# Performance work log

Measured on AMD Instinct MI355X. Metric: run time of the kernel, lower is better.

Reference implementation:

```python
import jax, jax.numpy as jnp
import numpy as np

SLOPE = 0.1
EPS = 1e-5


def setup_inputs() -> dict:
    key = jax.random.key(0)
    ks = jax.random.split(key, 12)
    C, INTER, RED = 256, 128, 32
    B, H, W = 8, 128, 128
    s = 0.05
    return {
        "x": jax.random.normal(ks[0], (B, C, H, W), jnp.float32),
        "se_w1": jax.random.normal(ks[1], (RED, C), jnp.float32) * s,
        "se_w2": jax.random.normal(ks[2], (C, RED), jnp.float32) * s,
        "wq": jax.random.normal(ks[3], (INTER, C), jnp.float32) * s,
        "bq": jax.random.normal(ks[4], (INTER,), jnp.float32) * s,
        "wk": jax.random.normal(ks[5], (INTER, C), jnp.float32) * s,
        "bk": jax.random.normal(ks[6], (INTER,), jnp.float32) * s,
        "wv": jax.random.normal(ks[7], (INTER, C), jnp.float32) * s,
        "bv": jax.random.normal(ks[8], (INTER,), jnp.float32) * s,
        "w_wg": jax.random.normal(ks[9], (INTER, INTER), jnp.float32) * s,
        "g_wg": jnp.ones((INTER,), jnp.float32),
        "be_wg": jnp.zeros((INTER,), jnp.float32),
        "rm_wg": jnp.zeros((INTER,), jnp.float32),
        "rv_wg": jnp.ones((INTER,), jnp.float32),
        "w_out": jax.random.normal(ks[10], (C, INTER), jnp.float32) * s,
        "b_out": jax.random.normal(ks[11], (C,), jnp.float32) * s,
        "g_out": jnp.ones((C,), jnp.float32),
        "be_out": jnp.zeros((C,), jnp.float32),
        "rm_out": jnp.zeros((C,), jnp.float32),
        "rv_out": jnp.ones((C,), jnp.float32),
    }


def _bn(x, g, b, rm, rv):
    # eval-mode batch norm over channel axis 1; x: [b, c, ...]
    shape = (1, -1) + (1,) * (x.ndim - 2)
    inv = g / jnp.sqrt(rv + EPS)
    return x * inv.reshape(shape) + (b - rm * inv).reshape(shape)


def reference(x, se_w1, se_w2, wq, bq, wk, bk, wv, bv,
              w_wg, g_wg, be_wg, rm_wg, rv_wg,
              w_out, b_out, g_out, be_out, rm_out, rv_out):
    B, C, H, W = x.shape
    # ---- Speactral_Attention (SE block) ----
    y = x.mean(axis=(2, 3))                                  # [b, c]
    y = jax.nn.leaky_relu(y @ se_w1.T, SLOPE)                # [b, c//8]
    y = jax.nn.sigmoid(y @ se_w2.T)                          # [b, c]
    xs = x * y[:, :, None, None]
    # ---- Spatial_GR ----
    xf = xs.reshape(B, C, H * W)                             # [b, c, n]
    q = jnp.einsum('ic,bcn->bin', wq, xf) + bq[None, :, None]
    k = jnp.einsum('ic,bcn->bin', wk, xf) + bk[None, :, None]
    v = jnp.einsum('ic,bcn->bin', wv, xf) + bv[None, :, None]
    # AV = softmax(q @ v^T) over last dim: [b, i, i]
    att = jax.nn.softmax(jnp.einsum('bin,bjn->bij', q, v), axis=2)
    # bmm(k^T, att) then transpose -> av[b,i,n] = sum_j att[b,j,i] * k[b,j,n]
    av = jnp.einsum('bji,bjn->bin', att, k)                  # [b, inter, n]
    avw = jnp.einsum('oi,bin->bon', w_wg, av)                # conv1d k=1, no bias
    avw = _bn(avw, g_wg, be_wg, rm_wg, rv_wg)
    out = jnp.einsum('co,bon->bcn', w_out, avw) + b_out[None, :, None]
    out = _bn(out.reshape(B, C, H, W), g_out, be_out, rm_out, rv_out)
    return jax.nn.leaky_relu(out + xs, SLOPE)
```

## Files before the change

### kernel.cpp

```cpp
#include <hip/hip_runtime.h>
#include <hip/hip_fp16.h>

#define NPIX 16384
#define CCH 256
#define INTR 128
#define REDD 32
#define NB 8
#define SLOPE 0.1f
#define BNEPS 1e-5f

typedef _Float16 f16x8 __attribute__((ext_vector_type(8)));
typedef __attribute__((ext_vector_type(16))) float f32x16;

#define OFF_GX    0
#define OFF_YM    524288
#define OFF_SC    526336
#define OFF_QS    530432
#define OFF_VS    531456
#define OFF_SWG   532480
#define OFF_TWG   532608
#define OFF_SOUT  532736
#define OFF_TOUT  532992
#define OFF_M     795392
#define OFF_W7    1450752
#define OFF_B6    1975040
#define OFF_XH    1977088
#define OFF_PART  18754304

__device__ __forceinline__ unsigned short h1(float f) {
    __half h = __float2half(f);
    return __half_as_ushort(h);
}

__device__ __forceinline__ uint4 cvt8h(const float4 a, const float4 c) {
    __half2 p0 = __floats2half2_rn(a.x, a.y);
    __half2 p1 = __floats2half2_rn(a.z, a.w);
    __half2 p2 = __floats2half2_rn(c.x, c.y);
    __half2 p3 = __floats2half2_rn(c.z, c.w);
    uint4 r;
    r.x = *(unsigned int*)&p0; r.y = *(unsigned int*)&p1;
    r.z = *(unsigned int*)&p2; r.w = *(unsigned int*)&p3;
    return r;
}

__device__ __forceinline__ f16x8 cvt8hf(const float4 a, const float4 c) {
    uint4 u = cvt8h(a, c);
    return *(f16x8*)&u;
}

__device__ __forceinline__ void gload_lds16(const void* g, void* l) {
    __builtin_amdgcn_global_load_lds((const __attribute__((address_space(1))) void*)g,
                                     (__attribute__((address_space(3))) void*)l, 16, 0, 0);
}

__global__ __launch_bounds__(256) void cvtrow_kernel(const float* __restrict__ x,
                                                     unsigned short* __restrict__ xh,
                                                     float* __restrict__ ymsum) {
    int row = blockIdx.x;
    const float4* p4 = (const float4*)(x + (size_t)row * NPIX);
    uint4* o4 = (uint4*)(xh + (size_t)row * NPIX);
    float s = 0.f;
    for (int i = threadIdx.x; i < NPIX / 8; i += 256) {
        float4 v0 = p4[2 * i];
        float4 v1 = p4[2 * i + 1];
        s += (v0.x + v0.y) + (v0.z + v0.w) + (v1.x + v1.y) + (v1.z + v1.w);
        o4[i] = cvt8h(v0, v1);
    }
    for (int off = 32; off > 0; off >>= 1) s += __shfl_xor(s, off);
    __shared__ float red[4];
    if ((threadIdx.x & 63) == 0) red[threadIdx.x >> 6] = s;
    __syncthreads();
    if (threadIdx.x == 0)
        ymsum[row] = red[0] + red[1] + red[2] + red[3];
}

__global__ __launch_bounds__(256) void head_kernel(const float* __restrict__ ymsum,
                                                   const float* __restrict__ se_w1,
                                                   const float* __restrict__ se_w2,
                                                   const float* __restrict__ wq,
                                                   const float* __restrict__ wv,
                                                   const float* __restrict__ g_wg, const float* __restrict__ be_wg,
                                                   const float* __restrict__ rm_wg, const float* __restrict__ rv_wg,
                                                   const float* __restrict__ g_out, const float* __restrict__ be_out,
                                                   const float* __restrict__ rm_out, const float* __restrict__ rv_out,
                                                   float* __restrict__ scale,
                                                   float* __restrict__ qs, float* __restrict__ vs,
                                                   float* __restrict__ swg, float* __restrict__ twg,
                                                   float* __restrict__ sout, float* __restrict__ tout) {
    int b = blockIdx.x, t = threadIdx.x;
    __shared__ float ys[CCH], y1s[REDD], rs[CCH];
    float ymr = ymsum[b * CCH + t];
    ys[t] = ymr * (1.f / 16384.f);
    if (b == 0) {
        if (t < INTR) {
            float s = g_wg[t] / sqrtf(rv_wg[t] + BNEPS);
            swg[t] = s;
            twg[t] = be_wg[t] - rm_wg[t] * s;
        }
        float s = g_out[t] / sqrtf(rv_out[t] + BNEPS);
        sout[t] = s;
        tout[t] = be_out[t] - rm_out[t] * s;
    }
    __syncthreads();
    if (t < REDD) {
        float a = 0.f;
        #pragma unroll 4
        for (int c = 0; c < CCH; ++c) a += se_w1[t * CCH + c] * ys[c];
        y1s[t] = a > 0.f ? a : SLOPE * a;
    }
    __syncthreads();
    float a = 0.f;
    #pragma unroll
    for (int r = 0; r < REDD; ++r) a += se_w2[t * REDD + r] * y1s[r];
    float sg = 1.f / (1.f + expf(-a));
    scale[b * CCH + t] = sg;
    rs[t] = sg * ymr;
    __syncthreads();
    const float* w = (t < INTR) ? (wq + t * CCH) : (wv + (t - INTR) * CCH);
    float a2 = 0.f;
    #pragma unroll 4
    for (int c = 0; c < CCH; ++c) a2 += w[c] * rs[c];
    if (t < INTR) qs[b * INTR + t] = a2;
    else          vs[b * INTR + (t - INTR)] = a2;
}

__global__ __launch_bounds__(256) void gram_partial_kernel(const unsigned short* __restrict__ xh,
                                                           unsigned short* __restrict__ partials,
                                                           int nch) {
    __shared__ __align__(16) unsigned short Ah[128 * 64];
    __shared__ __align__(16) unsigned short Bh[128 * 64];
    int bid = blockIdx.x;
    int chunk = bid % nch;
    int t2 = bid / nch;
    int tile = t2 % 3;
    int b = t2 / 3;
    int rowbase = (tile == 1) ? 128 : 0;
    int colbase = (tile == 0) ? 0 : 128;
    bool diag = (tile < 2);
    const unsigned short* xb = xh + (size_t)b * CCH * NPIX;
    int kpb = NPIX / nch;
    int n0 = chunk * kpb;
    int nsteps = kpb >> 6;
    int tid = threadIdx.x;
    int l = tid & 63, w = tid >> 6;
    int wrow = (w >> 1) * 64, wcol = (w & 1) * 64;
    int sr = l >> 3, ssg = l & 7;

    f32x16 acc[2][2];
    #pragma unroll
    for (int i = 0; i < 2; ++i)
        #pragma unroll
        for (int j = 0; j < 2; ++j)
            #pragma unroll
            for (int r = 0; r < 16; ++r) acc[i][j][r] = 0.f;

    for (int step = 0; step < nsteps; ++step) {
        int k0 = n0 + step * 64;
        __syncthreads();
        #pragma unroll
        for (int e = 0; e < 4; ++e) {
            int rbase = e * 32 + w * 8;
            int r = rbase + sr;
            int seg = ssg ^ (r & 7);
            gload_lds16(&xb[(size_t)(rowbase + r) * NPIX + k0 + seg * 8], &Ah[rbase * 64]);
            if (!diag)
                gload_lds16(&xb[(size_t)(colbase + r) * NPIX + k0 + seg * 8], &Bh[rbase * 64]);
        }
        __syncthreads();
        const unsigned short* BP = diag ? Ah : Bh;
        #pragma unroll
        for (int kk = 0; kk < 4; ++kk) {
            int useg = kk * 2 + (l >> 5);
            f16x8 af[2], bf[2];
            #pragma unroll
            for (int at = 0; at < 2; ++at) {
                int r = wrow + at * 32 + (l & 31);
                af[at] = *(const f16x8*)&Ah[r * 64 + ((useg ^ (r & 7)) << 3)];
            }
            #pragma unroll
            for (int bt = 0; bt < 2; ++bt) {
                int c = wcol + bt * 32 + (l & 31);
                bf[bt] = *(const f16x8*)&BP[c * 64 + ((useg ^ (c & 7)) << 3)];
            }
            #pragma unroll
            for (int at = 0; at < 2; ++at)
                #pragma unroll
                for (int bt = 0; bt < 2; ++bt)
                    acc[at][bt] = __builtin_amdgcn_mfma_f32_32x32x16_f16(af[at], bf[bt], acc[at][bt], 0, 0, 0);
        }
    }
    unsigned short* P = partials + (size_t)bid * (128 * 128);
    #pragma unroll
    for (int at = 0; at < 2; ++at)
        #pragma unroll
        for (int bt = 0; bt < 2; ++bt)
            #pragma unroll
            for (int r = 0; r < 16; ++r) {
                int lr = wrow + at * 32 + (r & 3) + ((r >> 2) << 3) + ((l >> 5) << 2);
                int lc = wcol + bt * 32 + (l & 31);
                P[lr * 128 + lc] = h1(acc[at][bt][r]);
            }
}

__global__ __launch_bounds__(256) void gram_reduce_kernel(const unsigned short* __restrict__ partials,
                                                          float* __restrict__ Gx,
                                                          int nch) {
    int bid = blockIdx.x;
    int part = bid & 15;
    int tileIdx = bid >> 4;
    int tile = tileIdx % 3;
    int b = tileIdx / 3;
    int rowbase = (tile == 1) ? 128 : 0;
    int colbase = (tile == 0) ? 0 : 128;
    int locIdx = part * 1024 + threadIdx.x * 4;
    const unsigned short* P = partials + (size_t)tileIdx * nch * (128 * 128) + locIdx;
    float4 s = make_float4(0.f, 0.f, 0.f, 0.f);
    for (int ch = 0; ch < nch; ++ch) {
        ushort4 v = *(const ushort4*)(P + (size_t)ch * (128 * 128));
        s.x += __half2float(__ushort_as_half(v.x));
        s.y += __half2float(__ushort_as_half(v.y));
        s.z += __half2float(__ushort_as_half(v.z));
        s.w += __half2float(__ushort_as_half(v.w));
    }
    int lr = locIdx >> 7, lc = locIdx & 127;
    float* G = Gx + (size_t)b * CCH * CCH;
    *(float4*)&G[(rowbase + lr) * CCH + colbase + lc] = s;
    if (tile == 2) {
        G[(colbase + lc + 0) * CCH + rowbase + lr] = s.x;
        G[(colbase + lc + 1) * CCH + rowbase + lr] = s.y;
        G[(colbase + lc + 2) * CCH + rowbase + lr] = s.z;
        G[(colbase + lc + 3) * CCH + rowbase + lr] = s.w;
    }
}

__global__ __launch_bounds__(256) void ts_kernel(const float* __restrict__ wq,
                                                 const float* __restrict__ scale,
                                                 const float* __restrict__ Gx,
                                                 const float* __restrict__ wv,
                                                 const float* __restrict__ bq,
                                                 const float* __restrict__ bv,
                                                 const float* __restrict__ qs,
                                                 const float* __restrict__ vs,
                                                 float* __restrict__ M) {
    int bid = blockIdx.x;
    int i = bid & 127, b = bid >> 7;
    int t = threadIdx.x;
    __shared__ float sw[CCH];
    __shared__ float t1s[CCH];
    __shared__ float part[256];
    __shared__ float redm[2], reds[2];
    sw[t] = wq[i * CCH + t] * scale[b * CCH + t];
    __syncthreads();
    const float* G = Gx + (size_t)b * CCH * CCH;
    float acc = 0.f;
    #pragma unroll 4
    for (int c = 0; c < CCH; ++c) acc += sw[c] * G[c * CCH + t];
    t1s[t] = acc * scale[b * CCH + t];
    __syncthreads();
    int j = t & 127, h = t >> 7;
    const float* wvr = wv + j * CCH + h * 128;
    const float* tp = t1s + h * 128;
    float p = 0.f;
    #pragma unroll 4
    for (int c = 0; c < 128; ++c) p += tp[c] * wvr[c];
    part[t] = p;
    __syncthreads();
    float acc2 = 0.f;
    if (t < 128)
        acc2 = part[t] + part[t + 128]
             + bq[i] * vs[b * INTR + j] + bv[j] * qs[b * INTR + i] + 16384.f * bq[i] * bv[j];
    float m = acc2;
    for (int off = 32; off > 0; off >>= 1) m = fmaxf(m, __shfl_xor(m, off));
    if (t == 0) redm[0] = m;
    if (t == 64) redm[1] = m;
    __syncthreads();
    m = fmaxf(redm[0], redm[1]);
    float e = expf(acc2 - m);
    float s = e;
    for (int off = 32; off > 0; off >>= 1) s += __shfl_xor(s, off);
    if (t == 0) reds[0] = s;
    if (t == 64) reds[1] = s;
    __syncthreads();
    s = reds[0] + reds[1];
    if (t < 128)
        M[(size_t)b * INTR * INTR + j * INTR + i] = e / s;
}

__global__ __launch_bounds__(256) void tail_kernel(const float* __restrict__ M,
                                                   const float* __restrict__ wk,
                                                   const float* __restrict__ bk,
                                                   const float* __restrict__ wwg,
                                                   const float* __restrict__ swg,
                                                   const float* __restrict__ twg,
                                                   const float* __restrict__ wout,
                                                   const float* __restrict__ bout,
                                                   const float* __restrict__ sout,
                                                   const float* __restrict__ tout,
                                                   const float* __restrict__ scale,
                                                   unsigned short* __restrict__ W7h,
                                                   float* __restrict__ b6) {
    __shared__ __align__(16) unsigned short Bt[256 * 128];
    __shared__ __align__(16) unsigned short Ot[256 * 128];
    __shared__ float bavS[INTR], b2S[INTR], scS[CCH], soS[CCH], swgS[INTR];
    int b = blockIdx.x, tid = threadIdx.x;
    int l = tid & 63, w = tid >> 6;
    const float* Mb = M + (size_t)b * INTR * INTR;

    scS[tid] = scale[b * CCH + tid];
    soS[tid] = sout[tid];
    if (tid < INTR) swgS[tid] = swg[tid];

    {
        int mn = tid & 63;
        int mk0 = tid >> 6;
        #pragma unroll
        for (int e = 0; e < 8; ++e) {
            int j0 = (mk0 + 4 * e) * 4;
            int c0 = mn * 4;
            float4 q0 = *(const float4*)&wk[(size_t)(j0 + 0) * CCH + c0];
            float4 q1 = *(const float4*)&wk[(size_t)(j0 + 1) * CCH + c0];
            float4 q2 = *(const float4*)&wk[(size_t)(j0 + 2) * CCH + c0];
            float4 q3 = *(const float4*)&wk[(size_t)(j0 + 3) * CCH + c0];
            int unit = j0 >> 3, sub = (j0 >> 2) & 1;
            int key = (c0 >> 2) & 7;
            #pragma unroll
            for (int jj = 0; jj < 4; ++jj) {
                float e0 = jj == 0 ? q0.x : jj == 1 ? q0.y : jj == 2 ? q0.z : q0.w;
                float e1 = jj == 0 ? q1.x : jj == 1 ? q1.y : jj == 2 ? q1.z : q1.w;
                float e2 = jj == 0 ? q2.x : jj == 1 ? q2.y : jj == 2 ? q2.z : q2.w;
                float e3 = jj == 0 ? q3.x : jj == 1 ? q3.y : jj == 2 ? q3.z : q3.w;
                ushort4 cv = make_ushort4(h1(e0), h1(e1), h1(e2), h1(e3));
                *(ushort4*)&Bt[(c0 + jj) * 128 + ((unit ^ key) << 3) + sub * 4] = cv;
            }
        }
    }
    if (tid < INTR) {
        float a = 0.f;
        #pragma unroll 4
        for (int j = 0; j < INTR; ++j) a += Mb[tid * INTR + j] * bk[j];
        bavS[tid] = a;
    }
    __syncthreads();

    {
        f32x16 acc[4][2];
        #pragma unroll
        for (int at = 0; at < 4; ++at)
            #pragma unroll
            for (int bt = 0; bt < 2; ++bt)
                #pragma unroll
                for (int r = 0; r < 16; ++r) acc[at][bt][r] = 0.f;
        #pragma unroll
        for (int kk = 0; kk < 8; ++kk) {
            int useg = kk * 2 + (l >> 5);
            f16x8 bf[2];
            #pragma unroll
            for (int bt = 0; bt < 2; ++bt) {
                int c = w * 64 + bt * 32 + (l & 31);
                bf[bt] = *(const f16x8*)&Bt[c * 128 + ((useg ^ ((c >> 2) & 7)) << 3)];
            }
            #pragma unroll
            for (int at = 0; at < 4; ++at) {
                int i = at * 32 + (l & 31);
                float4 a0 = *(const float4*)&Mb[(size_t)i * INTR + useg * 8];
                float4 a1 = *(const float4*)&Mb[(size_t)i * INTR + useg * 8 + 4];
                f16x8 af = cvt8hf(a0, a1);
                #pragma unroll
                for (int bt = 0; bt < 2; ++bt)
                    acc[at][bt] = __builtin_amdgcn_mfma_f32_32x32x16_f16(af, bf[bt], acc[at][bt], 0, 0, 0);
            }
        }
        if (tid < INTR) {
            float a = 0.f;
            #pragma unroll 4
            for (int i = 0; i < INTR; ++i) a += wwg[tid * INTR + i] * bavS[i];
            b2S[tid] = swgS[tid] * a + twg[tid];
        }
        __syncthreads();
        #pragma unroll
        for (int at = 0; at < 4; ++at)
            #pragma unroll
            for (int bt = 0; bt < 2; ++bt)
                #pragma unroll
                for (int r = 0; r < 16; ++r) {
                    int i = at * 32 + (r & 3) + ((r >> 2) << 3) + ((l >> 5) << 2);
                    int c = w * 64 + bt * 32 + (l & 31);
                    Ot[c * 128 + (((i >> 3) ^ ((c >> 2) & 7)) << 3) + (i & 7)] = h1(acc[at][bt][r]);
                }
    }
    __syncthreads();

    {
        f32x16 acc[4][2];
        #pragma unroll
        for (int at = 0; at < 4; ++at)
            #pragma unroll
            for (int bt = 0; bt < 2; ++bt)
                #pragma unroll
                for (int r = 0; r < 16; ++r) acc[at][bt][r] = 0.f;
        #pragma unroll
        for (int kk = 0; kk < 8; ++kk) {
            int useg = kk * 2 + (l >> 5);
            f16x8 bf[2];
            #pragma unroll
            for (int bt = 0; bt < 2; ++bt) {
                int c = w * 64 + bt * 32 + (l & 31);
                bf[bt] = *(const f16x8*)&Ot[c * 128 + ((useg ^ ((c >> 2) & 7)) << 3)];
            }
            #pragma unroll
            for (int at = 0; at < 4; ++at) {
                int o = at * 32 + (l & 31);
                float4 a0 = *(const float4*)&wwg[(size_t)o * INTR + useg * 8];
                float4 a1 = *(const float4*)&wwg[(size_t)o * INTR + useg * 8 + 4];
                f16x8 af = cvt8hf(a0, a1);
                #pragma unroll
                for (int bt = 0; bt < 2; ++bt)
                    acc[at][bt] = __builtin_amdgcn_mfma_f32_32x32x16_f16(af, bf[bt], acc[at][bt], 0, 0, 0);
            }
        }
        {
            float a = 0.f;
            #pragma unroll 4
            for (int o = 0; o < INTR; ++o) a += wout[tid * INTR + o] * b2S[o];
            float b5 = a + bout[tid];
            b6[b * CCH + tid] = soS[tid] * b5 + tout[tid];
        }
        __syncthreads();
        #pragma unroll
        for (int at = 0; at < 4; ++at)
            #pragma unroll
            for (int bt = 0; bt < 2; ++bt)
                #pragma unroll
                for (int r = 0; r < 16; ++r) {
                    int o = at * 32 + (r & 3) + ((r >> 2) << 3) + ((l >> 5) << 2);
                    int c = w * 64 + bt * 32 + (l & 31);
                    Bt[c * 128 + (((o >> 3) ^ ((c >> 2) & 7)) << 3) + (o & 7)] = h1(swgS[o] * acc[at][bt][r]);
                }
    }
    __syncthreads();

    unsigned short* Wb = W7h + (size_t)b * CCH * CCH;
    #pragma unroll
    for (int p = 0; p < 2; ++p) {
        f32x16 acc[4][2];
        #pragma unroll
        for (int at = 0; at < 4; ++at)
            #pragma unroll
            for (int bt = 0; bt < 2; ++bt)
                #pragma unroll
                for (int r = 0; r < 16; ++r) acc[at][bt][r] = 0.f;
        #pragma unroll
        for (int kk = 0; kk < 8; ++kk) {
            int useg = kk * 2 + (l >> 5);
            f16x8 bf[2];
            #pragma unroll
            for (int bt = 0; bt < 2; ++bt) {
                int cp = w * 64 + bt * 32 + (l & 31);
                bf[bt] = *(const f16x8*)&Bt[cp * 128 + ((useg ^ ((cp >> 2) & 7)) << 3)];
            }
            #pragma unroll
            for (int at = 0; at < 4; ++at) {
                int cc = p * 128 + at * 32 + (l & 31);
                float4 a0 = *(const float4*)&wout[(size_t)cc * INTR + useg * 8];
                float4 a1 = *(const float4*)&wout[(size_t)cc * INTR + useg * 8 + 4];
                f16x8 af = cvt8hf(a0, a1);
                #pragma unroll
                for (int bt = 0; bt < 2; ++bt)
                    acc[at][bt] = __builtin_amdgcn_mfma_f32_32x32x16_f16(af, bf[bt], acc[at][bt], 0, 0, 0);
            }
        }
        #pragma unroll
        for (int at = 0; at < 4; ++at)
            #pragma unroll
            for (int bt = 0; bt < 2; ++bt)
                #pragma unroll
                for (int r = 0; r < 16; ++r) {
                    int c = p * 128 + at * 32 + (r & 3) + ((r >> 2) << 3) + ((l >> 5) << 2);
                    int cp = w * 64 + bt * 32 + (l & 31);
                    float w6 = soS[c] * acc[at][bt][r] + ((c == cp) ? 1.f : 0.f);
                    Wb[c * CCH + cp] = h1(w6 * scS[cp]);
                }
    }
}

__global__ __launch_bounds__(256, 4) void final_mfma_kernel(const unsigned short* __restrict__ W7h,
                                                            const unsigned short* __restrict__ xh,
                                                            const float* __restrict__ b6,
                                                            float* __restrict__ out) {
    __shared__ __align__(16) unsigned short Ws[128 * 64];
    __shared__ __align__(16) unsigned short Xs[128 * 64];
    int bid0 = blockIdx.x;
    int bid = (bid0 & 7) * 256 + (bid0 >> 3);
    int ct = bid & 1;
    int nt = (bid >> 1) & 127;
    int b = bid >> 8;
    int cbase = ct * 128, n0 = nt * 128;
    const unsigned short* xb = xh + (size_t)b * CCH * NPIX;
    const unsigned short* Wb = W7h + (size_t)b * CCH * CCH;
    int tid = threadIdx.x;
    int l = tid & 63, w = tid >> 6;
    int wrow = (w >> 1) * 64, wcol = (w & 1) * 64;
    int mn = tid & 31, mk0 = tid >> 5;
    int sr = l >> 3, ssg = l & 7;

    f32x16 acc[2][2];
    #pragma unroll
    for (int i = 0; i < 2; ++i)
        #pragma unroll
        for (int j = 0; j < 2; ++j)
            #pragma unroll
            for (int r = 0; r < 16; ++r) acc[i][j][r] = 0.f;

    for (int step = 0; step < 4; ++step) {
        int k0 = step * 64;
        __syncthreads();
        #pragma unroll
        for (int e = 0; e < 4; ++e) {
            int rbase = e * 32 + w * 8;
            int r = rbase + sr;
            int seg = ssg ^ (r & 7);
            gload_lds16(&Wb[(size_t)(cbase + r) * CCH + k0 + seg * 8], &Ws[rbase * 64]);
        }
        #pragma unroll
        for (int mi = 0; mi < 2; ++mi) {
            int mk = mk0 + mi * 8;
            const unsigned short* sp = &xb[(size_t)(k0 + mk * 4) * NPIX + n0 + mn * 4];
            ushort4 q0 = *(const ushort4*)sp;
            ushort4 q1 = *(const ushort4*)(sp + NPIX);
            ushort4 q2 = *(const ushort4*)(sp + 2 * NPIX);
            ushort4 q3 = *(const ushort4*)(sp + 3 * NPIX);
            int klo = mk * 4;
            int unit = klo >> 3, sub = (klo & 7) >> 2;
            #pragma unroll
            for (int j = 0; j < 4; ++j) {
                unsigned short e0 = j == 0 ? q0.x : j == 1 ? q0.y : j == 2 ? q0.z : q0.w;
                unsigned short e1 = j == 0 ? q1.x : j == 1 ? q1.y : j == 2 ? q1.z : q1.w;
                unsigned short e2 = j == 0 ? q2.x : j == 1 ? q2.y : j == 2 ? q2.z : q2.w;
                unsigned short e3 = j == 0 ? q3.x : j == 1 ? q3.y : j == 2 ? q3.z : q3.w;
                int nl = mn * 4 + j;
                ushort4 cv = make_ushort4(e0, e1, e2, e3);
                int idx = nl * 64 + ((unit ^ ((nl >> 2) & 7)) << 3) + sub * 4;
                *(ushort4*)&Xs[idx] = cv;
            }
        }
        __syncthreads();
        #pragma unroll
        for (int kk = 0; kk < 4; ++kk) {
            int useg = kk * 2 + (l >> 5);
            f16x8 af[2], bfr[2];
            #pragma unroll
            for (int at = 0; at < 2; ++at) {
                int c = wrow + at * 32 + (l & 31);
                af[at] = *(const f16x8*)&Ws[c * 64 + ((useg ^ (c & 7)) << 3)];
            }
            #pragma unroll
            for (int bt = 0; bt < 2; ++bt) {
                int n = wcol + bt * 32 + (l & 31);
                bfr[bt] = *(const f16x8*)&Xs[n * 64 + ((useg ^ ((n >> 2) & 7)) << 3)];
            }
            #pragma unroll
            for (int at = 0; at < 2; ++at)
                #pragma unroll
                for (int bt = 0; bt < 2; ++bt)
                    acc[at][bt] = __builtin_amdgcn_mfma_f32_32x32x16_f16(af[at], bfr[bt], acc[at][bt], 0, 0, 0);
        }
    }
    #pragma unroll
    for (int at = 0; at < 2; ++at)
        #pragma unroll
        for (int bt = 0; bt < 2; ++bt)
            #pragma unroll
            for (int r = 0; r < 16; ++r) {
                int c = cbase + wrow + at * 32 + (r & 3) + ((r >> 2) << 3) + ((l >> 5) << 2);
                int n = n0 + wcol + bt * 32 + (l & 31);
                float v = acc[at][bt][r] + b6[b * CCH + c];
                v = v > 0.f ? v : SLOPE * v;
                out[(size_t)b * CCH * NPIX + (size_t)c * NPIX + n] = v;
            }
}

extern "C" void kernel_launch(void* const* d_in, const int* in_sizes, int n_in,
                              void* d_out, int out_size, void* d_ws, size_t ws_size,
                              hipStream_t stream) {
    (void)in_sizes; (void)n_in; (void)out_size;
    const float* x      = (const float*)d_in[0];
    const float* se_w1  = (const float*)d_in[1];
    const float* se_w2  = (const float*)d_in[2];
    const float* wq     = (const float*)d_in[3];
    const float* bq     = (const float*)d_in[4];
    const float* wk     = (const float*)d_in[5];
    const float* bk     = (const float*)d_in[6];
    const float* wv     = (const float*)d_in[7];
    const float* bv     = (const float*)d_in[8];
    const float* w_wg   = (const float*)d_in[9];
    const float* w_out  = (const float*)d_in[14];
    const float* b_out  = (const float*)d_in[15];
    float* out = (float*)d_out;
    float* ws = (float*)d_ws;
    unsigned short* xh = (unsigned short*)(ws + OFF_XH);

    size_t avail = ws_size / sizeof(float);
    int nch = 32;
    while (nch > 1 && (size_t)OFF_PART + (size_t)NB * 3 * nch * 8192 > avail) nch >>= 1;

    cvtrow_kernel<<<NB * CCH, 256, 0, stream>>>(x, xh, ws + OFF_YM);
    gram_partial_kernel<<<NB * 3 * nch, 256, 0, stream>>>(xh, (unsigned short*)(ws + OFF_PART), nch);
    gram_reduce_kernel<<<NB * 3 * 16, 256, 0, stream>>>((const unsigned short*)(ws + OFF_PART),
                                                        ws + OFF_GX, nch);
    head_kernel<<<NB, 256, 0, stream>>>(ws + OFF_YM, se_w1, se_w2, wq, wv,
                                        (const float*)d_in[10], (const float*)d_in[11],
                                        (const float*)d_in[12], (const float*)d_in[13],
                                        (const float*)d_in[16], (const float*)d_in[17],
                                        (const float*)d_in[18], (const float*)d_in[19],
                                        ws + OFF_SC, ws + OFF_QS, ws + OFF_VS,
                                        ws + OFF_SWG, ws + OFF_TWG, ws + OFF_SOUT, ws + OFF_TOUT);
    ts_kernel<<<NB * INTR, 256, 0, stream>>>(wq, ws + OFF_SC, ws + OFF_GX, wv, bq, bv,
                                             ws + OFF_QS, ws + OFF_VS, ws + OFF_M);
    tail_kernel<<<NB, 256, 0, stream>>>(ws + OFF_M, wk, bk, w_wg, ws + OFF_SWG, ws + OFF_TWG,
                                        w_out, b_out, ws + OFF_SOUT, ws + OFF_TOUT, ws + OFF_SC,
                                        (unsigned short*)(ws + OFF_W7), ws + OFF_B6);
    final_mfma_kernel<<<NB * 2 * 128, 256, 0, stream>>>((const unsigned short*)(ws + OFF_W7),
                                                        xh, ws + OFF_B6, out);
}
```

Baseline: 234.3 us.

## Double-buffer LDS tiles in gram and final MFMA kernels

Adds LDS double buffering to the gram partial kernel and the final MFMA kernel. The next K-slice is prefetched, via direct-to-LDS loads or register-staged X loads, while MFMAs run on the current buffer, which is meant to hide global memory latency. The final kernel drops its occupancy hint of 4 blocks per CU. The gram split count goes from 32 to 64 chunks. Doubling LDS per block may lower occupancy, and the larger partial buffer adds reduce traffic.

```diff
diff --git a/kernel.cpp b/kernel.cpp
--- a/kernel.cpp
+++ b/kernel.cpp
@@ -127,8 +127,8 @@
 __global__ __launch_bounds__(256) void gram_partial_kernel(const unsigned short* __restrict__ xh,
                                                            unsigned short* __restrict__ partials,
                                                            int nch) {
-    __shared__ __align__(16) unsigned short Ah[128 * 64];
-    __shared__ __align__(16) unsigned short Bh[128 * 64];
+    __shared__ __align__(16) unsigned short Ah[2 * 128 * 64];
+    __shared__ __align__(16) unsigned short Bh[2 * 128 * 64];
     int bid = blockIdx.x;
     int chunk = bid % nch;
     int t2 = bid / nch;
@@ -154,20 +154,36 @@
             #pragma unroll
             for (int r = 0; r < 16; ++r) acc[i][j][r] = 0.f;
 
-    for (int step = 0; step < nsteps; ++step) {
-        int k0 = n0 + step * 64;
-        __syncthreads();
+    {
         #pragma unroll
         for (int e = 0; e < 4; ++e) {
             int rbase = e * 32 + w * 8;
             int r = rbase + sr;
             int seg = ssg ^ (r & 7);
-            gload_lds16(&xb[(size_t)(rowbase + r) * NPIX + k0 + seg * 8], &Ah[rbase * 64]);
+            gload_lds16(&xb[(size_t)(rowbase + r) * NPIX + n0 + seg * 8], &Ah[rbase * 64]);
             if (!diag)
-                gload_lds16(&xb[(size_t)(colbase + r) * NPIX + k0 + seg * 8], &Bh[rbase * 64]);
-        }
+                gload_lds16(&xb[(size_t)(colbase + r) * NPIX + n0 + seg * 8], &Bh[rbase * 64]);
+        }
+    }
+    int cur = 0;
+    for (int step = 0; step < nsteps; ++step) {
         __syncthreads();
-        const unsigned short* BP = diag ? Ah : Bh;
+        if (step + 1 < nsteps) {
+            int kn = n0 + (step + 1) * 64;
+            unsigned short* AhN = Ah + (cur ^ 1) * 8192;
+            unsigned short* BhN = Bh + (cur ^ 1) * 8192;
+            #pragma unroll
+            for (int e = 0; e < 4; ++e) {
+                int rbase = e * 32 + w * 8;
+                int r = rbase + sr;
+                int seg = ssg ^ (r & 7);
+                gload_lds16(&xb[(size_t)(rowbase + r) * NPIX + kn + seg * 8], &AhN[rbase * 64]);
+                if (!diag)
+                    gload_lds16(&xb[(size_t)(colbase + r) * NPIX + kn + seg * 8], &BhN[rbase * 64]);
+            }
+        }
+        const unsigned short* AP = Ah + cur * 8192;
+        const unsigned short* BP = diag ? AP : (Bh + cur * 8192);
         #pragma unroll
         for (int kk = 0; kk < 4; ++kk) {
             int useg = kk * 2 + (l >> 5);
@@ -175,7 +191,7 @@
             #pragma unroll
             for (int at = 0; at < 2; ++at) {
                 int r = wrow + at * 32 + (l & 31);
-                af[at] = *(const f16x8*)&Ah[r * 64 + ((useg ^ (r & 7)) << 3)];
+                af[at] = *(const f16x8*)&AP[r * 64 + ((useg ^ (r & 7)) << 3)];
             }
             #pragma unroll
             for (int bt = 0; bt < 2; ++bt) {
@@ -188,6 +204,7 @@
                 for (int bt = 0; bt < 2; ++bt)
                     acc[at][bt] = __builtin_amdgcn_mfma_f32_32x32x16_f16(af[at], bf[bt], acc[at][bt], 0, 0, 0);
         }
+        cur ^= 1;
     }
     unsigned short* P = partials + (size_t)bid * (128 * 128);
     #pragma unroll
@@ -483,12 +500,47 @@
     }
 }
 
-__global__ __launch_bounds__(256, 4) void final_mfma_kernel(const unsigned short* __restrict__ W7h,
-                                                            const unsigned short* __restrict__ xh,
-                                                            const float* __restrict__ b6,
-                                                            float* __restrict__ out) {
-    __shared__ __align__(16) unsigned short Ws[128 * 64];
-    __shared__ __align__(16) unsigned short Xs[128 * 64];
+__device__ __forceinline__ void final_loadX(const unsigned short* xb, int k0, int n0,
+                                            int mn, int mk0, ushort4 xq[2][4]) {
+    #pragma unroll
+    for (int mi = 0; mi < 2; ++mi) {
+        int mk = mk0 + mi * 8;
+        const unsigned short* sp = &xb[(size_t)(k0 + mk * 4) * NPIX + n0 + mn * 4];
+        xq[mi][0] = *(const ushort4*)sp;
+        xq[mi][1] = *(const ushort4*)(sp + NPIX);
+        xq[mi][2] = *(const ushort4*)(sp + 2 * NPIX);
+        xq[mi][3] = *(const ushort4*)(sp + 3 * NPIX);
+    }
+}
+
+__device__ __forceinline__ void final_writeX(unsigned short* XsB, int mn, int mk0,
+                                             const ushort4 xq[2][4]) {
+    #pragma unroll
+    for (int mi = 0; mi < 2; ++mi) {
+        int mk = mk0 + mi * 8;
+        ushort4 q0 = xq[mi][0], q1 = xq[mi][1], q2 = xq[mi][2], q3 = xq[mi][3];
+        int klo = mk * 4;
+        int unit = klo >> 3, sub = (klo & 7) >> 2;
+        #pragma unroll
+        for (int j = 0; j < 4; ++j) {
+            unsigned short e0 = j == 0 ? q0.x : j == 1 ? q0.y : j == 2 ? q0.z : q0.w;
+            unsigned short e1 = j == 0 ? q1.x : j == 1 ? q1.y : j == 2 ? q1.z : q1.w;
+            unsigned short e2 = j == 0 ? q2.x : j == 1 ? q2.y : j == 2 ? q2.z : q2.w;
+            unsigned short e3 = j == 0 ? q3.x : j == 1 ? q3.y : j == 2 ? q3.z : q3.w;
+            int nl = mn * 4 + j;
+            ushort4 cv = make_ushort4(e0, e1, e2, e3);
+            int idx = nl * 64 + ((unit ^ ((nl >> 2) & 7)) << 3) + sub * 4;
+            *(ushort4*)&XsB[idx] = cv;
+        }
+    }
+}
+
+__global__ __launch_bounds__(256) void final_mfma_kernel(const unsigned short* __restrict__ W7h,
+                                                         const unsigned short* __restrict__ xh,
+                                                         const float* __restrict__ b6,
+                                                         float* __restrict__ out) {
+    __shared__ __align__(16) unsigned short Ws[2 * 128 * 64];
+    __shared__ __align__(16) unsigned short Xs[2 * 128 * 64];
     int bid0 = blockIdx.x;
     int bid = (bid0 & 7) * 256 + (bid0 >> 3);
     int ct = bid & 1;
@@ -511,39 +563,36 @@
             #pragma unroll
             for (int r = 0; r < 16; ++r) acc[i][j][r] = 0.f;
 
-    for (int step = 0; step < 4; ++step) {
-        int k0 = step * 64;
-        __syncthreads();
+    ushort4 xq[2][4];
+    {
         #pragma unroll
         for (int e = 0; e < 4; ++e) {
             int rbase = e * 32 + w * 8;
             int r = rbase + sr;
             int seg = ssg ^ (r & 7);
-            gload_lds16(&Wb[(size_t)(cbase + r) * CCH + k0 + seg * 8], &Ws[rbase * 64]);
-        }
-        #pragma unroll
-        for (int mi = 0; mi < 2; ++mi) {
-            int mk = mk0 + mi * 8;
-            const unsigned short* sp = &xb[(size_t)(k0 + mk * 4) * NPIX + n0 + mn * 4];
-            ushort4 q0 = *(const ushort4*)sp;
-            ushort4 q1 = *(const ushort4*)(sp + NPIX);
-            ushort4 q2 = *(const ushort4*)(sp + 2 * NPIX);
-            ushort4 q3 = *(const ushort4*)(sp + 3 * NPIX);
-            int klo = mk * 4;
-            int unit = klo >> 3, sub = (klo & 7) >> 2;
-            #pragma unroll
-            for (int j = 0; j < 4; ++j) {
-                unsigned short e0 = j == 0 ? q0.x : j == 1 ? q0.y : j == 2 ? q0.z : q0.w;
-                unsigned short e1 = j == 0 ? q1.x : j == 1 ? q1.y : j == 2 ? q1.z : q1.w;
-                unsigned short e2 = j == 0 ? q2.x : j == 1 ? q2.y : j == 2 ? q2.z : q2.w;
-                unsigned short e3 = j == 0 ? q3.x : j == 1 ? q3.y : j == 2 ? q3.z : q3.w;
-                int nl = mn * 4 + j;
-                ushort4 cv = make_ushort4(e0, e1, e2, e3);
-                int idx = nl * 64 + ((unit ^ ((nl >> 2) & 7)) << 3) + sub * 4;
-                *(ushort4*)&Xs[idx] = cv;
-            }
-        }
+            gload_lds16(&Wb[(size_t)(cbase + r) * CCH + seg * 8], &Ws[rbase * 64]);
+        }
+        final_loadX(xb, 0, n0, mn, mk0, xq);
+        final_writeX(Xs, mn, mk0, xq);
+    }
+    int cur = 0;
+    for (int step = 0; step < 4; ++step) {
         __syncthreads();
+        bool pf = (step < 3);
+        int kn = (step + 1) * 64;
+        if (pf) {
+            unsigned short* WsN = Ws + (cur ^ 1) * 8192;
+            #pragma unroll
+            for (int e = 0; e < 4; ++e) {
+                int rbase = e * 32 + w * 8;
+                int r = rbase + sr;
+                int seg = ssg ^ (r & 7);
+                gload_lds16(&Wb[(size_t)(cbase + r) * CCH + kn + seg * 8], &WsN[rbase * 64]);
+            }
+            final_loadX(xb, kn, n0, mn, mk0, xq);
+        }
+        const unsigned short* WsC = Ws + cur * 8192;
+        const unsigned short* XsC = Xs + cur * 8192;
         #pragma unroll
         for (int kk = 0; kk < 4; ++kk) {
             int useg = kk * 2 + (l >> 5);
@@ -551,12 +600,12 @@
             #pragma unroll
             for (int at = 0; at < 2; ++at) {
                 int c = wrow + at * 32 + (l & 31);
-                af[at] = *(const f16x8*)&Ws[c * 64 + ((useg ^ (c & 7)) << 3)];
+                af[at] = *(const f16x8*)&WsC[c * 64 + ((useg ^ (c & 7)) << 3)];
             }
             #pragma unroll
             for (int bt = 0; bt < 2; ++bt) {
                 int n = wcol + bt * 32 + (l & 31);
-                bfr[bt] = *(const f16x8*)&Xs[n * 64 + ((useg ^ ((n >> 2) & 7)) << 3)];
+                bfr[bt] = *(const f16x8*)&XsC[n * 64 + ((useg ^ ((n >> 2) & 7)) << 3)];
             }
             #pragma unroll
             for (int at = 0; at < 2; ++at)
@@ -564,6 +613,8 @@
                 for (int bt = 0; bt < 2; ++bt)
                     acc[at][bt] = __builtin_amdgcn_mfma_f32_32x32x16_f16(af[at], bfr[bt], acc[at][bt], 0, 0, 0);
         }
+        if (pf) final_writeX(Xs + (cur ^ 1) * 8192, mn, mk0, xq);
+        cur ^= 1;
     }
     #pragma unroll
     for (int at = 0; at < 2; ++at)
@@ -600,7 +651,7 @@
     unsigned short* xh = (unsigned short*)(ws + OFF_XH);
 
     size_t avail = ws_size / sizeof(float);
-    int nch = 32;
+    int nch = 64;
     while (nch > 1 && (size_t)OFF_PART + (size_t)NB * 3 * nch * 8192 > avail) nch >>= 1;
 
     cvtrow_kernel<<<NB * CCH, 256, 0, stream>>>(x, xh, ws + OFF_YM);
```

Result: slower. 252.8 us (+7.9%).
